# Optimization experiments

Hardware: AMD Instinct MI355X
Metric: run time of the kernel (lower is better)

## Reference

```python
import jax, jax.numpy as jnp
import numpy as np

B, N, M = 64, 4096, 128
TOTAL_LABELS = 21
TOTAL_POS = 128
TOTAL_NEG = 128
VARIANCES = jnp.array([0.1, 0.1, 0.2, 0.2], dtype=jnp.float32)


def _make_boxes(key, b, n):
    # valid [y1, x1, y2, x2] boxes in [0, 1]
    k1, k2 = jax.random.split(key)
    c1 = jax.random.uniform(k1, (b, n, 2), dtype=jnp.float32)
    c2 = jax.random.uniform(k2, (b, n, 2), dtype=jnp.float32)
    lo = jnp.minimum(c1, c2)
    hi = jnp.maximum(c1, c2)
    return jnp.concatenate([lo, hi], axis=-1)


def setup_inputs() -> dict:
    key = jax.random.key(0)
    k1, k2, k3 = jax.random.split(key, 3)
    roi_bboxes = _make_boxes(k1, B, N)
    gt_boxes = _make_boxes(k2, B, M)
    gt_labels = jax.random.randint(k3, (B, M), 0, TOTAL_LABELS, dtype=jnp.int32)
    return {"roi_bboxes": roi_bboxes, "gt_boxes": gt_boxes, "gt_labels": gt_labels}


def generate_iou(bboxes, gt_boxes):
    # bboxes: [B,N,4], gt_boxes: [B,M,4]; format [y1,x1,y2,x2] -> iou [B,N,M]
    by1, bx1, by2, bx2 = jnp.split(bboxes, 4, axis=-1)      # each [B,N,1]
    gy1, gx1, gy2, gx2 = jnp.split(gt_boxes, 4, axis=-1)    # each [B,M,1]
    gt_area = ((gy2 - gy1) * (gx2 - gx1))[..., 0]           # [B,M]
    bbox_area = ((by2 - by1) * (bx2 - bx1))[..., 0]         # [B,N]
    x_top = jnp.maximum(bx1, jnp.swapaxes(gx1, 1, 2))       # [B,N,M]
    y_top = jnp.maximum(by1, jnp.swapaxes(gy1, 1, 2))
    x_bot = jnp.minimum(bx2, jnp.swapaxes(gx2, 1, 2))
    y_bot = jnp.minimum(by2, jnp.swapaxes(gy2, 1, 2))
    inter = jnp.maximum(x_bot - x_top, 0.0) * jnp.maximum(y_bot - y_top, 0.0)
    union = bbox_area[:, :, None] + gt_area[:, None, :] - inter
    return inter / union


def randomly_select_mask(key, mask, count):
    # keep at most `count` True entries per row, chosen at random (rpn_utils.randomly_select_xyz_mask)
    rand = jax.random.randint(key, mask.shape, 1, count * 10, dtype=jnp.int32)
    mult = mask.astype(jnp.int32) * rand
    order = jnp.argsort(-mult, axis=1)       # descending sort of masked random scores
    rank = jnp.argsort(order, axis=1)        # rank of each element in that order
    return mask & (rank < count)


def bbox_to_delta(bboxes, gt_boxes):
    bw = bboxes[..., 3] - bboxes[..., 1]
    bh = bboxes[..., 2] - bboxes[..., 0]
    bcx = bboxes[..., 1] + 0.5 * bw
    bcy = bboxes[..., 0] + 0.5 * bh
    gw = gt_boxes[..., 3] - gt_boxes[..., 1]
    gh = gt_boxes[..., 2] - gt_boxes[..., 0]
    gcx = gt_boxes[..., 1] + 0.5 * gw
    gcy = gt_boxes[..., 0] + 0.5 * gh
    bw = jnp.where(bw == 0.0, 1e-3, bw)
    bh = jnp.where(bh == 0.0, 1e-3, bh)
    dx = (gcx - bcx) / bw
    dy = (gcy - bcy) / bh
    gw_safe = jnp.where(gw == 0.0, 1.0, gw)  # avoid nan grads through masked log
    gh_safe = jnp.where(gh == 0.0, 1.0, gh)
    dw = jnp.where(gw == 0.0, 0.0, jnp.log(gw_safe / bw))
    dh = jnp.where(gh == 0.0, 0.0, jnp.log(gh_safe / bh))
    return jnp.stack([dy, dx, dh, dw], axis=-1)


def _forward(roi_bboxes, gt_boxes, gt_labels):
    kp, kn = jax.random.split(jax.random.key(42))
    iou_map = generate_iou(roi_bboxes, gt_boxes)             # [B,N,M]
    max_idx = jnp.argmax(iou_map, axis=2)                    # [B,N]
    merged = jnp.max(iou_map, axis=2)                        # [B,N]
    pos_mask = randomly_select_mask(kp, merged > 0.5, TOTAL_POS)
    neg_mask = randomly_select_mask(kn, (merged < 0.5) & (merged > 0.1), TOTAL_NEG)
    # batched gather of best-matching gt box / label per roi
    gt_boxes_map = jnp.take_along_axis(gt_boxes, max_idx[..., None], axis=1)   # [B,N,4]
    gt_labels_map = jnp.take_along_axis(gt_labels, max_idx, axis=1)            # [B,N]
    expanded_gt_boxes = jnp.where(pos_mask[..., None], gt_boxes_map, 0.0)
    pos_gt_labels = jnp.where(pos_mask, gt_labels_map, -1)
    expanded_gt_labels = pos_gt_labels  # hyper_params['background'] == False
    deltas = bbox_to_delta(roi_bboxes, expanded_gt_boxes) / VARIANCES           # [B,N,4]
    labels_oh = jax.nn.one_hot(expanded_gt_labels, TOTAL_LABELS, dtype=deltas.dtype)  # [B,N,L]; -1 -> all zeros
    roi_bbox_deltas = labels_oh[..., None] * deltas[..., None, :]               # [B,N,L,4]
    return roi_bbox_deltas, labels_oh


def reference(roi_bboxes, gt_boxes, gt_labels):
    return _forward(roi_bboxes, gt_boxes, gt_labels)
```

## Files before the change

kernel.cpp:

```cpp
#include <hip/hip_runtime.h>
#include <stdint.h>

#pragma clang fp contract(off)


#define BB 64
#define NN 4096
#define MM 128
#define LL 21
#define NTOT (BB * NN)
#define DELTA_ELEMS ((size_t)BB * NN * LL * 4)

__host__ __device__ __forceinline__ uint32_t rotl32(uint32_t v, int s) {
  return (v << s) | (v >> (32 - s));
}

__host__ __device__ inline void threefry2x32(uint32_t k0, uint32_t k1,
                                             uint32_t x0, uint32_t x1,
                                             uint32_t* o0, uint32_t* o1) {
  const uint32_t ks2 = k0 ^ k1 ^ 0x1BD11BDAu;
  x0 += k0; x1 += k1;
#define TF_R(r) do { x0 += x1; x1 = rotl32(x1, (r)); x1 ^= x0; } while (0)
  TF_R(13); TF_R(15); TF_R(26); TF_R(6);
  x0 += k1;  x1 += ks2 + 1u;
  TF_R(17); TF_R(29); TF_R(16); TF_R(24);
  x0 += ks2; x1 += k0 + 2u;
  TF_R(13); TF_R(15); TF_R(26); TF_R(6);
  x0 += k0;  x1 += k1 + 3u;
  TF_R(17); TF_R(29); TF_R(16); TF_R(24);
  x0 += k1;  x1 += ks2 + 4u;
  TF_R(13); TF_R(15); TF_R(26); TF_R(6);
  x0 += ks2; x1 += k0 + 5u;
#undef TF_R
  *o0 = x0; *o1 = x1;
}

__device__ __forceinline__ uint32_t jax_bits32(uint32_t ka, uint32_t kb, uint32_t idx) {
  uint32_t o0, o1;
  threefry2x32(ka, kb, 0u, idx, &o0, &o1);
  return o0 ^ o1;
}

__device__ __forceinline__ uint32_t jax_randint_1_1280(uint32_t k1a, uint32_t k1b,
                                                       uint32_t k2a, uint32_t k2b,
                                                       uint32_t idx) {
  const uint32_t hi = jax_bits32(k1a, k1b, idx);
  const uint32_t lo = jax_bits32(k2a, k2b, idx);
  const uint32_t off = ((hi % 1279u) * 882u + (lo % 1279u)) % 1279u;
  return 1u + off;
}

__device__ __forceinline__ float4 compute_delta(const float4 r, const float4 g) {
  float bh = r.z - r.x, bw = r.w - r.y;
  const float bcy = r.x + 0.5f * bh, bcx = r.y + 0.5f * bw;
  const float gh = g.z - g.x, gw = g.w - g.y;
  const float gcy = g.x + 0.5f * gh, gcx = g.y + 0.5f * gw;
  if (bw == 0.0f) bw = 1e-3f;
  if (bh == 0.0f) bh = 1e-3f;
  const float dx = (gcx - bcx) / bw;
  const float dy = (gcy - bcy) / bh;
  const float dw = (gw == 0.0f) ? 0.0f : logf(gw / bw);
  const float dh = (gh == 0.0f) ? 0.0f : logf(gh / bh);
  float4 dv;
  dv.x = dy / 0.1f; dv.y = dx / 0.1f; dv.z = dh / 0.2f; dv.w = dw / 0.2f;
  return dv;
}

__global__ __launch_bounds__(256) void iou_pack_kernel(
    const float* __restrict__ roi, const float* __restrict__ gt,
    uint32_t* __restrict__ packed,
    uint32_t k1a, uint32_t k1b, uint32_t k2a, uint32_t k2b) {
  __shared__ float4 gtb[MM];
  __shared__ float gar[MM];
  const int b = blockIdx.y;
  const int t = threadIdx.x;
  if (t < MM) {
    const float4 g = ((const float4*)gt)[b * MM + t];
    gtb[t] = g;
    gar[t] = (g.z - g.x) * (g.w - g.y);
  }
  __syncthreads();
  const int i = b * NN + blockIdx.x * 256 + t;
  const float4 r = ((const float4*)roi)[i];
  const float barea = (r.z - r.x) * (r.w - r.y);
  float best = -1.0f;
  int bm = 0;
  for (int m = 0; m < MM; ++m) {
    const float4 g = gtb[m];
    const float xt = fmaxf(r.y, g.y);
    const float yt = fmaxf(r.x, g.x);
    const float xb = fminf(r.w, g.w);
    const float yb = fminf(r.z, g.z);
    const float inter = fmaxf(xb - xt, 0.0f) * fmaxf(yb - yt, 0.0f);
    const float uni = (barea + gar[m]) - inter;
    const float iou = inter / uni;
    if (iou > best) { best = iou; bm = m; }
  }
  const uint32_t rnd = jax_randint_1_1280(k1a, k1b, k2a, k2b, (uint32_t)i);
  packed[i] = (uint32_t)bm | ((best > 0.5f) ? (rnd << 7) : 0u);
}

__global__ __launch_bounds__(256) void fused_out_kernel(
    const float* __restrict__ roi, const float* __restrict__ gt,
    const int* __restrict__ glab, const uint32_t* __restrict__ packed,
    float* __restrict__ out) {
  __shared__ uint32_t hist[1280];
  __shared__ uint32_t scan[256];
  __shared__ unsigned char selb[NN];
  __shared__ float4 sdv[256];
  __shared__ int slbl[256];
  __shared__ int s_thr;
  __shared__ int s_take;
  const int br = blockIdx.x;
  const int b = br >> 4;
  const int win0 = (br & 15) << 8;
  const int t = threadIdx.x;
  for (int j = t; j < 1280; j += 256) hist[j] = 0u;
  if (t == 0) { s_thr = 0; s_take = 0; }
  __syncthreads();

  uint32_t rv[16];
  const uint4* p4 = (const uint4*)(packed + (size_t)b * NN);
  #pragma unroll
  for (int q = 0; q < 4; ++q) {
    const uint4 w = p4[t * 4 + q];
    rv[q * 4 + 0] = w.x >> 7;
    rv[q * 4 + 1] = w.y >> 7;
    rv[q * 4 + 2] = w.z >> 7;
    rv[q * 4 + 3] = w.w >> 7;
  }
  #pragma unroll
  for (int k = 0; k < 16; ++k)
    if (rv[k]) atomicAdd(&hist[rv[k]], 1u);
  __syncthreads();

  uint32_t chunk = 0;
  #pragma unroll
  for (int j = 0; j < 5; ++j) chunk += hist[t * 5 + j];
  scan[t] = chunk;
  __syncthreads();
  for (int off = 1; off < 256; off <<= 1) {
    const uint32_t v = (t + off < 256) ? scan[t + off] : 0u;
    __syncthreads();
    scan[t] += v;
    __syncthreads();
  }
  const uint32_t total = scan[0];
  if (total > 128u) {
    const uint32_t Sc = scan[t];
    const uint32_t Sn = (t < 255) ? scan[t + 1] : 0u;
    if (Sc >= 128u && Sn < 128u) {
      uint32_t s = Sn;
      #pragma unroll
      for (int j = 4; j >= 0; --j) {
        const uint32_t h = hist[t * 5 + j];
        if (s + h >= 128u) { s_thr = t * 5 + j; s_take = 128 - (int)s; break; }
        s += h;
      }
    }
  }
  __syncthreads();
  const uint32_t thr = (uint32_t)s_thr;
  const uint32_t take = (uint32_t)s_take;

  uint32_t lt = 0;
  if (thr > 0) {
    #pragma unroll
    for (int k = 0; k < 16; ++k) lt += (rv[k] == thr) ? 1u : 0u;
  }
  scan[t] = lt;
  __syncthreads();
  for (int off = 1; off < 256; off <<= 1) {
    const uint32_t v = (t >= off) ? scan[t - off] : 0u;
    __syncthreads();
    scan[t] += v;
    __syncthreads();
  }
  uint32_t run = scan[t] - lt;
  uint32_t sw0 = 0, sw1 = 0, sw2 = 0, sw3 = 0;
  #pragma unroll
  for (int k = 0; k < 16; ++k) {
    bool s;
    if (thr == 0) {
      s = rv[k] > 0u;
    } else {
      s = (rv[k] > thr);
      if (rv[k] == thr) { s = (run < take); ++run; }
    }
    const uint32_t bit = s ? 1u : 0u;
    if (k < 4)       sw0 |= bit << (k * 8);
    else if (k < 8)  sw1 |= bit << ((k - 4) * 8);
    else if (k < 12) sw2 |= bit << ((k - 8) * 8);
    else             sw3 |= bit << ((k - 12) * 8);
  }
  ((uint4*)selb)[t] = make_uint4(sw0, sw1, sw2, sw3);
  __syncthreads();

  const int irow = win0 + t;
  const int i = b * NN + irow;
  float4 dv = {0.f, 0.f, 0.f, 0.f};
  int lbl = -1;
  if (selb[irow]) {
    const int mi = (int)(packed[i] & 127u);
    const float4 r = ((const float4*)roi)[i];
    const float4 g = ((const float4*)gt)[b * MM + mi];
    lbl = glab[b * MM + mi];
    dv = compute_delta(r, g);
  }
  sdv[t] = dv;
  slbl[t] = lbl;
  __syncthreads();
  const float4 z = {0.f, 0.f, 0.f, 0.f};
  const size_t ri0 = (size_t)b * NN + win0;
  float4* dbase = (float4*)out + ri0 * LL;
  #pragma unroll
  for (int k = 0; k < LL; ++k) {
    const int q = t + k * 256;
    const int r = q / 21;
    const int f = q - r * 21;
    dbase[q] = (f == slbl[r]) ? sdv[r] : z;
  }
  float4* lbase = (float4*)(out + DELTA_ELEMS) + ri0 * LL / 4;
  for (int q = t; q < 1344; q += 256) {
    const int e0 = q * 4;
    float4 v;
    const int r0 = e0 / 21;       v.x = ((e0 - r0 * 21) == slbl[r0]) ? 1.f : 0.f;
    const int r1 = (e0 + 1) / 21; v.y = ((e0 + 1 - r1 * 21) == slbl[r1]) ? 1.f : 0.f;
    const int r2 = (e0 + 2) / 21; v.z = ((e0 + 2 - r2 * 21) == slbl[r2]) ? 1.f : 0.f;
    const int r3 = (e0 + 3) / 21; v.w = ((e0 + 3 - r3 * 21) == slbl[r3]) ? 1.f : 0.f;
    lbase[q] = v;
  }
}

__global__ __launch_bounds__(256) void iou_kernel_s(const float* __restrict__ roi,
                                                    const float* __restrict__ gt,
                                                    int* __restrict__ midx,
                                                    float* __restrict__ merged) {
  __shared__ float4 gtb[MM];
  __shared__ float gar[MM];
  const int b = blockIdx.y;
  const int t = threadIdx.x;
  if (t < MM) {
    const float4 g = ((const float4*)gt)[b * MM + t];
    gtb[t] = g;
    gar[t] = (g.z - g.x) * (g.w - g.y);
  }
  __syncthreads();
  const int i = b * NN + blockIdx.x * 256 + t;
  const float4 r = ((const float4*)roi)[i];
  const float barea = (r.z - r.x) * (r.w - r.y);
  float best = -1.0f;
  int bm = 0;
  for (int m = 0; m < MM; ++m) {
    const float4 g = gtb[m];
    const float xt = fmaxf(r.y, g.y);
    const float yt = fmaxf(r.x, g.x);
    const float xb = fminf(r.w, g.w);
    const float yb = fminf(r.z, g.z);
    const float inter = fmaxf(xb - xt, 0.0f) * fmaxf(yb - yt, 0.0f);
    const float iou = inter / ((barea + gar[m]) - inter);
    if (iou > best) { best = iou; bm = m; }
  }
  midx[(size_t)i * 84] = bm;
  merged[(size_t)i * 84] = best;
}

__global__ __launch_bounds__(256) void select_kernel_s(const float* __restrict__ merged,
                                                       int* __restrict__ sel,
                                                       uint32_t k1a, uint32_t k1b,
                                                       uint32_t k2a, uint32_t k2b) {
  __shared__ uint32_t buf[NN];
  __shared__ uint32_t hist[1280];
  __shared__ uint32_t scan[256];
  __shared__ int s_thr;
  __shared__ int s_take;
  const int b = blockIdx.x;
  const int t = threadIdx.x;
  for (int j = t; j < 1280; j += 256) hist[j] = 0u;
  if (t == 0) { s_thr = 0; s_take = 0; }
  #pragma unroll
  for (int k = 0; k < 16; ++k) {
    const int li = t + k * 256;
    buf[li] = __float_as_uint(merged[(size_t)(b * NN + li) * 84]);
  }
  __syncthreads();
  uint32_t rv[16];
  const int lbase = t * 16;
  #pragma unroll
  for (int k = 0; k < 16; ++k) {
    const int li = lbase + k;
    uint32_t r = 0u;
    if (__uint_as_float(buf[li]) > 0.5f) {
      r = jax_randint_1_1280(k1a, k1b, k2a, k2b, (uint32_t)(b * NN + li));
      atomicAdd(&hist[r], 1u);
    }
    rv[k] = r;
  }
  __syncthreads();
  uint32_t chunk = 0;
  #pragma unroll
  for (int j = 0; j < 5; ++j) chunk += hist[t * 5 + j];
  scan[t] = chunk;
  __syncthreads();
  for (int off = 1; off < 256; off <<= 1) {
    const uint32_t v = (t + off < 256) ? scan[t + off] : 0u;
    __syncthreads();
    scan[t] += v;
    __syncthreads();
  }
  const uint32_t total = scan[0];
  if (total > 128u) {
    const uint32_t Sc = scan[t];
    const uint32_t Sn = (t < 255) ? scan[t + 1] : 0u;
    if (Sc >= 128u && Sn < 128u) {
      uint32_t s = Sn;
      #pragma unroll
      for (int j = 4; j >= 0; --j) {
        const uint32_t h = hist[t * 5 + j];
        if (s + h >= 128u) { s_thr = t * 5 + j; s_take = 128 - (int)s; break; }
        s += h;
      }
    }
  }
  __syncthreads();
  const int thr = s_thr;
  const uint32_t take = (uint32_t)s_take;
  uint32_t lt = 0;
  if (thr > 0) {
    #pragma unroll
    for (int k = 0; k < 16; ++k) lt += (rv[k] == (uint32_t)thr) ? 1u : 0u;
  }
  scan[t] = lt;
  __syncthreads();
  for (int off = 1; off < 256; off <<= 1) {
    const uint32_t v = (t >= off) ? scan[t - off] : 0u;
    __syncthreads();
    scan[t] += v;
    __syncthreads();
  }
  uint32_t run = scan[t] - lt;
  #pragma unroll
  for (int k = 0; k < 16; ++k) {
    bool s;
    if (thr == 0) {
      s = rv[k] > 0u;
    } else {
      s = (rv[k] > (uint32_t)thr);
      if (rv[k] == (uint32_t)thr) { s = (run < take); ++run; }
    }
    buf[lbase + k] = s ? 1u : 0u;
  }
  __syncthreads();
  #pragma unroll
  for (int k = 0; k < 16; ++k) {
    const int li = t + k * 256;
    sel[(size_t)(b * NN + li) * 84] = (int)buf[li];
  }
}

__global__ __launch_bounds__(256) void out_kernel_s(const float* __restrict__ roi,
                                                    const float* __restrict__ gt,
                                                    const int* __restrict__ glab,
                                                    const int* __restrict__ midx,
                                                    const int* __restrict__ sel,
                                                    float* __restrict__ out) {
  __shared__ float4 sdv[256];
  __shared__ int slbl[256];
  const int t = threadIdx.x;
  const int ri0 = blockIdx.x * 256;
  const int i = ri0 + t;
  const int b = i >> 12;
  const int mi = midx[(size_t)i * 84];
  const int sv = sel[(size_t)i * 84];
  float4 dv = {0.f, 0.f, 0.f, 0.f};
  int lbl = -1;
  if (sv) {
    const float4 r = ((const float4*)roi)[i];
    const float4 g = ((const float4*)gt)[b * MM + mi];
    lbl = glab[b * MM + mi];
    dv = compute_delta(r, g);
  }
  sdv[t] = dv;
  slbl[t] = lbl;
  __syncthreads();
  const float4 z = {0.f, 0.f, 0.f, 0.f};
  float4* dbase = (float4*)out + (size_t)ri0 * LL;
  #pragma unroll
  for (int k = 0; k < LL; ++k) {
    const int q = t + k * 256;
    const int r = q / 21;
    const int f = q - r * 21;
    dbase[q] = (f == slbl[r]) ? sdv[r] : z;
  }
  float4* lbase = (float4*)(out + DELTA_ELEMS) + (size_t)ri0 * LL / 4;
  for (int q = t; q < 1344; q += 256) {
    const int e0 = q * 4;
    float4 v;
    const int r0 = e0 / 21;       v.x = ((e0 - r0 * 21) == slbl[r0]) ? 1.f : 0.f;
    const int r1 = (e0 + 1) / 21; v.y = ((e0 + 1 - r1 * 21) == slbl[r1]) ? 1.f : 0.f;
    const int r2 = (e0 + 2) / 21; v.z = ((e0 + 2 - r2 * 21) == slbl[r2]) ? 1.f : 0.f;
    const int r3 = (e0 + 3) / 21; v.w = ((e0 + 3 - r3 * 21) == slbl[r3]) ? 1.f : 0.f;
    lbase[q] = v;
  }
}

extern "C" void kernel_launch(void* const* d_in, const int* in_sizes, int n_in,
                              void* d_out, int out_size, void* d_ws, size_t ws_size,
                              hipStream_t stream) {
  const float* roi = (const float*)d_in[0];
  const float* gt  = (const float*)d_in[1];
  const int* glab  = (const int*)d_in[2];
  float* out = (float*)d_out;

  uint32_t kp0, kp1, k1a, k1b, k2a, k2b;
  threefry2x32(0u, 42u, 0u, 0u, &kp0, &kp1);
  threefry2x32(kp0, kp1, 0u, 0u, &k1a, &k1b);
  threefry2x32(kp0, kp1, 0u, 1u, &k2a, &k2b);

  if (d_ws != nullptr && ws_size >= (size_t)NTOT * 4) {
    uint32_t* packed = (uint32_t*)d_ws;
    hipLaunchKernelGGL(iou_pack_kernel, dim3(NN / 256, BB), dim3(256), 0, stream,
                       roi, gt, packed, k1a, k1b, k2a, k2b);
    hipLaunchKernelGGL(fused_out_kernel, dim3(NTOT / 256), dim3(256), 0, stream,
                       roi, gt, glab, packed, out);
  } else {
    int* midx     = (int*)out;
    float* merged = out + 1;
    int* sel      = (int*)out + 2;
    hipLaunchKernelGGL(iou_kernel_s, dim3(NN / 256, BB), dim3(256), 0, stream,
                       roi, gt, midx, merged);
    hipLaunchKernelGGL(select_kernel_s, dim3(BB), dim3(256), 0, stream,
                       merged, sel, k1a, k1b, k2a, k2b);
    hipLaunchKernelGGL(out_kernel_s, dim3(NTOT / 256), dim3(256), 0, stream,
                       roi, gt, glab, midx, sel, out);
  }
}
```

Before: 57.52 us.

## Use wavefront shuffle scans and hoist loads and delta compute in fused kernel

The two shared-memory Hillis-Steele scans in the selection kernel, each with a barrier at every step, become wavefront shuffle scans plus a small per-wave combine, which cuts the number of block-wide barriers. Global loads of the packed words, the roi, the gt box and the label are issued at kernel start and the delta is computed for every row before selection, so the memory latency overlaps the histogram phase. In the IoU kernels the gt area is recomputed in registers instead of being read from a shared array, and the inner loop is unrolled. The cost is extra arithmetic for rows that end up unselected, plus extra gather loads for those rows.

```diff
diff --git a/kernel.cpp b/kernel.cpp
--- a/kernel.cpp
+++ b/kernel.cpp
@@ -71,29 +71,25 @@
     uint32_t* __restrict__ packed,
     uint32_t k1a, uint32_t k1b, uint32_t k2a, uint32_t k2b) {
   __shared__ float4 gtb[MM];
-  __shared__ float gar[MM];
   const int b = blockIdx.y;
   const int t = threadIdx.x;
-  if (t < MM) {
-    const float4 g = ((const float4*)gt)[b * MM + t];
-    gtb[t] = g;
-    gar[t] = (g.z - g.x) * (g.w - g.y);
-  }
-  __syncthreads();
   const int i = b * NN + blockIdx.x * 256 + t;
   const float4 r = ((const float4*)roi)[i];
+  if (t < MM) gtb[t] = ((const float4*)gt)[b * MM + t];
+  __syncthreads();
   const float barea = (r.z - r.x) * (r.w - r.y);
   float best = -1.0f;
   int bm = 0;
+  #pragma unroll 4
   for (int m = 0; m < MM; ++m) {
     const float4 g = gtb[m];
+    const float garea = (g.z - g.x) * (g.w - g.y);
     const float xt = fmaxf(r.y, g.y);
     const float yt = fmaxf(r.x, g.x);
     const float xb = fminf(r.w, g.w);
     const float yb = fminf(r.z, g.z);
     const float inter = fmaxf(xb - xt, 0.0f) * fmaxf(yb - yt, 0.0f);
-    const float uni = (barea + gar[m]) - inter;
-    const float iou = inter / uni;
+    const float iou = inter / ((barea + garea) - inter);
     if (iou > best) { best = iou; bm = m; }
   }
   const uint32_t rnd = jax_randint_1_1280(k1a, k1b, k2a, k2b, (uint32_t)i);
@@ -105,7 +101,8 @@
     const int* __restrict__ glab, const uint32_t* __restrict__ packed,
     float* __restrict__ out) {
   __shared__ uint32_t hist[1280];
-  __shared__ uint32_t scan[256];
+  __shared__ uint32_t scan[257];
+  __shared__ uint32_t wsum[4];
   __shared__ unsigned char selb[NN];
   __shared__ float4 sdv[256];
   __shared__ int slbl[256];
@@ -115,40 +112,62 @@
   const int b = br >> 4;
   const int win0 = (br & 15) << 8;
   const int t = threadIdx.x;
+  const int lane = t & 63;
+  const int wid = t >> 6;
+
+  const int irow = win0 + t;
+  const int i = b * NN + irow;
+  const uint32_t pk_own = packed[i];
+  const uint4* p4 = (const uint4*)(packed + (size_t)b * NN);
+  const uint4 w0 = p4[t * 4 + 0];
+  const uint4 w1 = p4[t * 4 + 1];
+  const uint4 w2 = p4[t * 4 + 2];
+  const uint4 w3 = p4[t * 4 + 3];
+  const float4 r = ((const float4*)roi)[i];
+
   for (int j = t; j < 1280; j += 256) hist[j] = 0u;
-  if (t == 0) { s_thr = 0; s_take = 0; }
+  if (t == 0) { s_thr = 0; s_take = 0; scan[256] = 0u; }
   __syncthreads();
 
   uint32_t rv[16];
-  const uint4* p4 = (const uint4*)(packed + (size_t)b * NN);
-  #pragma unroll
-  for (int q = 0; q < 4; ++q) {
-    const uint4 w = p4[t * 4 + q];
-    rv[q * 4 + 0] = w.x >> 7;
-    rv[q * 4 + 1] = w.y >> 7;
-    rv[q * 4 + 2] = w.z >> 7;
-    rv[q * 4 + 3] = w.w >> 7;
-  }
+  rv[0] = w0.x >> 7;  rv[1] = w0.y >> 7;  rv[2] = w0.z >> 7;  rv[3] = w0.w >> 7;
+  rv[4] = w1.x >> 7;  rv[5] = w1.y >> 7;  rv[6] = w1.z >> 7;  rv[7] = w1.w >> 7;
+  rv[8] = w2.x >> 7;  rv[9] = w2.y >> 7;  rv[10] = w2.z >> 7; rv[11] = w2.w >> 7;
+  rv[12] = w3.x >> 7; rv[13] = w3.y >> 7; rv[14] = w3.z >> 7; rv[15] = w3.w >> 7;
   #pragma unroll
   for (int k = 0; k < 16; ++k)
     if (rv[k]) atomicAdd(&hist[rv[k]], 1u);
+
+  const int mi = (int)(pk_own & 127u);
+  const float4 g = ((const float4*)gt)[b * MM + mi];
+  int lbl = glab[b * MM + mi];
+  float4 dv = compute_delta(r, g);
   __syncthreads();
 
   uint32_t chunk = 0;
   #pragma unroll
   for (int j = 0; j < 5; ++j) chunk += hist[t * 5 + j];
-  scan[t] = chunk;
-  __syncthreads();
-  for (int off = 1; off < 256; off <<= 1) {
-    const uint32_t v = (t + off < 256) ? scan[t + off] : 0u;
-    __syncthreads();
-    scan[t] += v;
-    __syncthreads();
-  }
+  uint32_t v = chunk;
+  #pragma unroll
+  for (int off = 1; off < 64; off <<= 1) {
+    const uint32_t u = __shfl_down(v, off);
+    if (lane + off < 64) v += u;
+  }
+  if (lane == 0) wsum[wid] = v;
+  __syncthreads();
+  {
+    uint32_t add = 0;
+    #pragma unroll
+    for (int w = 0; w < 4; ++w)
+      if (w > wid) add += wsum[w];
+    v += add;
+  }
+  scan[t] = v;
+  __syncthreads();
   const uint32_t total = scan[0];
   if (total > 128u) {
-    const uint32_t Sc = scan[t];
-    const uint32_t Sn = (t < 255) ? scan[t + 1] : 0u;
+    const uint32_t Sc = v;
+    const uint32_t Sn = scan[t + 1];
     if (Sc >= 128u && Sn < 128u) {
       uint32_t s = Sn;
       #pragma unroll
@@ -168,15 +187,19 @@
     #pragma unroll
     for (int k = 0; k < 16; ++k) lt += (rv[k] == thr) ? 1u : 0u;
   }
-  scan[t] = lt;
-  __syncthreads();
-  for (int off = 1; off < 256; off <<= 1) {
-    const uint32_t v = (t >= off) ? scan[t - off] : 0u;
-    __syncthreads();
-    scan[t] += v;
-    __syncthreads();
-  }
-  uint32_t run = scan[t] - lt;
+  uint32_t p = lt;
+  #pragma unroll
+  for (int off = 1; off < 64; off <<= 1) {
+    const uint32_t u = __shfl_up(p, off);
+    if (lane >= off) p += u;
+  }
+  if (lane == 63) wsum[wid] = p;
+  __syncthreads();
+  uint32_t run = p - lt;
+  #pragma unroll
+  for (int w = 0; w < 4; ++w)
+    if (w < wid) run += wsum[w];
+
   uint32_t sw0 = 0, sw1 = 0, sw2 = 0, sw3 = 0;
   #pragma unroll
   for (int k = 0; k < 16; ++k) {
@@ -196,17 +219,7 @@
   ((uint4*)selb)[t] = make_uint4(sw0, sw1, sw2, sw3);
   __syncthreads();
 
-  const int irow = win0 + t;
-  const int i = b * NN + irow;
-  float4 dv = {0.f, 0.f, 0.f, 0.f};
-  int lbl = -1;
-  if (selb[irow]) {
-    const int mi = (int)(packed[i] & 127u);
-    const float4 r = ((const float4*)roi)[i];
-    const float4 g = ((const float4*)gt)[b * MM + mi];
-    lbl = glab[b * MM + mi];
-    dv = compute_delta(r, g);
-  }
+  if (!selb[irow]) lbl = -1;
   sdv[t] = dv;
   slbl[t] = lbl;
   __syncthreads();
@@ -216,19 +229,19 @@
   #pragma unroll
   for (int k = 0; k < LL; ++k) {
     const int q = t + k * 256;
-    const int r = q / 21;
-    const int f = q - r * 21;
-    dbase[q] = (f == slbl[r]) ? sdv[r] : z;
+    const int rr = q / 21;
+    const int f = q - rr * 21;
+    dbase[q] = (f == slbl[rr]) ? sdv[rr] : z;
   }
   float4* lbase = (float4*)(out + DELTA_ELEMS) + ri0 * LL / 4;
   for (int q = t; q < 1344; q += 256) {
     const int e0 = q * 4;
-    float4 v;
-    const int r0 = e0 / 21;       v.x = ((e0 - r0 * 21) == slbl[r0]) ? 1.f : 0.f;
-    const int r1 = (e0 + 1) / 21; v.y = ((e0 + 1 - r1 * 21) == slbl[r1]) ? 1.f : 0.f;
-    const int r2 = (e0 + 2) / 21; v.z = ((e0 + 2 - r2 * 21) == slbl[r2]) ? 1.f : 0.f;
-    const int r3 = (e0 + 3) / 21; v.w = ((e0 + 3 - r3 * 21) == slbl[r3]) ? 1.f : 0.f;
-    lbase[q] = v;
+    float4 vv;
+    const int r0 = e0 / 21;       vv.x = ((e0 - r0 * 21) == slbl[r0]) ? 1.f : 0.f;
+    const int r1 = (e0 + 1) / 21; vv.y = ((e0 + 1 - r1 * 21) == slbl[r1]) ? 1.f : 0.f;
+    const int r2 = (e0 + 2) / 21; vv.z = ((e0 + 2 - r2 * 21) == slbl[r2]) ? 1.f : 0.f;
+    const int r3 = (e0 + 3) / 21; vv.w = ((e0 + 3 - r3 * 21) == slbl[r3]) ? 1.f : 0.f;
+    lbase[q] = vv;
   }
 }
 
@@ -237,14 +250,9 @@
                                                     int* __restrict__ midx,
                                                     float* __restrict__ merged) {
   __shared__ float4 gtb[MM];
-  __shared__ float gar[MM];
   const int b = blockIdx.y;
   const int t = threadIdx.x;
-  if (t < MM) {
-    const float4 g = ((const float4*)gt)[b * MM + t];
-    gtb[t] = g;
-    gar[t] = (g.z - g.x) * (g.w - g.y);
-  }
+  if (t < MM) gtb[t] = ((const float4*)gt)[b * MM + t];
   __syncthreads();
   const int i = b * NN + blockIdx.x * 256 + t;
   const float4 r = ((const float4*)roi)[i];
@@ -253,12 +261,13 @@
   int bm = 0;
   for (int m = 0; m < MM; ++m) {
     const float4 g = gtb[m];
+    const float garea = (g.z - g.x) * (g.w - g.y);
     const float xt = fmaxf(r.y, g.y);
     const float yt = fmaxf(r.x, g.x);
     const float xb = fminf(r.w, g.w);
     const float yb = fminf(r.z, g.z);
     const float inter = fmaxf(xb - xt, 0.0f) * fmaxf(yb - yt, 0.0f);
-    const float iou = inter / ((barea + gar[m]) - inter);
+    const float iou = inter / ((barea + garea) - inter);
     if (iou > best) { best = iou; bm = m; }
   }
   midx[(size_t)i * 84] = bm;
```

After: 57.58 us. Within noise of the previous version (+0.1%).

## Zero outputs in IoU kernel and scatter only selected rows per batch

Applied to the files above, without the earlier changes.

The IoU/pack kernel now also writes zeros over the whole delta and one-hot output regions, so the dense write overlaps with the IoU compute. The second kernel runs one block per batch, does the random selection once instead of 16 times, and scatters deltas and the 1.0 label only for the selected rows. This removes the redundant per-window histogram/select work and the dense masked output pass. The risk is that the scatter kernel has only 64 blocks. Any unselected row relies entirely on the earlier zero fill, which is ordered correctly on the same stream. The fallback IoU kernel now recomputes gt area inline rather than caching it in shared memory.

```diff
diff --git a/kernel.cpp b/kernel.cpp
--- a/kernel.cpp
+++ b/kernel.cpp
@@ -66,22 +66,34 @@
   return dv;
 }
 
-__global__ __launch_bounds__(256) void iou_pack_kernel(
+__global__ __launch_bounds__(256) void iou_zero_pack_kernel(
     const float* __restrict__ roi, const float* __restrict__ gt,
-    uint32_t* __restrict__ packed,
+    uint32_t* __restrict__ packed, float* __restrict__ out,
     uint32_t k1a, uint32_t k1b, uint32_t k2a, uint32_t k2b) {
   __shared__ float4 gtb[MM];
   __shared__ float gar[MM];
   const int b = blockIdx.y;
   const int t = threadIdx.x;
+  const int ri0 = blockIdx.x * 256;
+  const int i = b * NN + ri0 + t;
+  const float4 r = ((const float4*)roi)[i];
   if (t < MM) {
     const float4 g = ((const float4*)gt)[b * MM + t];
     gtb[t] = g;
     gar[t] = (g.z - g.x) * (g.w - g.y);
   }
   __syncthreads();
-  const int i = b * NN + blockIdx.x * 256 + t;
-  const float4 r = ((const float4*)roi)[i];
+
+  const float4 z = {0.f, 0.f, 0.f, 0.f};
+  const size_t gri0 = (size_t)b * NN + ri0;
+  float4* dbase = (float4*)out + gri0 * LL;
+  #pragma unroll
+  for (int k = 0; k < LL; ++k) dbase[t + k * 256] = z;
+  float4* lbase = (float4*)(out + DELTA_ELEMS) + gri0 * LL / 4;
+  #pragma unroll
+  for (int q = 0; q < 5; ++q) lbase[t + q * 256] = z;
+  if (t < 1344 - 5 * 256) lbase[t + 5 * 256] = z;
+
   const float barea = (r.z - r.x) * (r.w - r.y);
   float best = -1.0f;
   int bm = 0;
@@ -100,20 +112,15 @@
   packed[i] = (uint32_t)bm | ((best > 0.5f) ? (rnd << 7) : 0u);
 }
 
-__global__ __launch_bounds__(256) void fused_out_kernel(
+__global__ __launch_bounds__(256) void select_scatter_kernel(
     const float* __restrict__ roi, const float* __restrict__ gt,
     const int* __restrict__ glab, const uint32_t* __restrict__ packed,
     float* __restrict__ out) {
   __shared__ uint32_t hist[1280];
   __shared__ uint32_t scan[256];
-  __shared__ unsigned char selb[NN];
-  __shared__ float4 sdv[256];
-  __shared__ int slbl[256];
   __shared__ int s_thr;
   __shared__ int s_take;
-  const int br = blockIdx.x;
-  const int b = br >> 4;
-  const int win0 = (br & 15) << 8;
+  const int b = blockIdx.x;
   const int t = threadIdx.x;
   for (int j = t; j < 1280; j += 256) hist[j] = 0u;
   if (t == 0) { s_thr = 0; s_take = 0; }
@@ -177,7 +184,7 @@
     __syncthreads();
   }
   uint32_t run = scan[t] - lt;
-  uint32_t sw0 = 0, sw1 = 0, sw2 = 0, sw3 = 0;
+
   #pragma unroll
   for (int k = 0; k < 16; ++k) {
     bool s;
@@ -187,48 +194,16 @@
       s = (rv[k] > thr);
       if (rv[k] == thr) { s = (run < take); ++run; }
     }
-    const uint32_t bit = s ? 1u : 0u;
-    if (k < 4)       sw0 |= bit << (k * 8);
-    else if (k < 8)  sw1 |= bit << ((k - 4) * 8);
-    else if (k < 12) sw2 |= bit << ((k - 8) * 8);
-    else             sw3 |= bit << ((k - 12) * 8);
-  }
-  ((uint4*)selb)[t] = make_uint4(sw0, sw1, sw2, sw3);
-  __syncthreads();
-
-  const int irow = win0 + t;
-  const int i = b * NN + irow;
-  float4 dv = {0.f, 0.f, 0.f, 0.f};
-  int lbl = -1;
-  if (selb[irow]) {
-    const int mi = (int)(packed[i] & 127u);
-    const float4 r = ((const float4*)roi)[i];
-    const float4 g = ((const float4*)gt)[b * MM + mi];
-    lbl = glab[b * MM + mi];
-    dv = compute_delta(r, g);
-  }
-  sdv[t] = dv;
-  slbl[t] = lbl;
-  __syncthreads();
-  const float4 z = {0.f, 0.f, 0.f, 0.f};
-  const size_t ri0 = (size_t)b * NN + win0;
-  float4* dbase = (float4*)out + ri0 * LL;
-  #pragma unroll
-  for (int k = 0; k < LL; ++k) {
-    const int q = t + k * 256;
-    const int r = q / 21;
-    const int f = q - r * 21;
-    dbase[q] = (f == slbl[r]) ? sdv[r] : z;
-  }
-  float4* lbase = (float4*)(out + DELTA_ELEMS) + ri0 * LL / 4;
-  for (int q = t; q < 1344; q += 256) {
-    const int e0 = q * 4;
-    float4 v;
-    const int r0 = e0 / 21;       v.x = ((e0 - r0 * 21) == slbl[r0]) ? 1.f : 0.f;
-    const int r1 = (e0 + 1) / 21; v.y = ((e0 + 1 - r1 * 21) == slbl[r1]) ? 1.f : 0.f;
-    const int r2 = (e0 + 2) / 21; v.z = ((e0 + 2 - r2 * 21) == slbl[r2]) ? 1.f : 0.f;
-    const int r3 = (e0 + 3) / 21; v.w = ((e0 + 3 - r3 * 21) == slbl[r3]) ? 1.f : 0.f;
-    lbase[q] = v;
+    if (s) {
+      const int i = b * NN + t * 16 + k;
+      const int mi = (int)(packed[i] & 127u);
+      const float4 r = ((const float4*)roi)[i];
+      const float4 g = ((const float4*)gt)[b * MM + mi];
+      const int lbl = glab[b * MM + mi];
+      const float4 dv = compute_delta(r, g);
+      ((float4*)out)[(size_t)i * LL + lbl] = dv;
+      out[DELTA_ELEMS + (size_t)i * LL + lbl] = 1.0f;
+    }
   }
 }
 
@@ -237,14 +212,9 @@
                                                     int* __restrict__ midx,
                                                     float* __restrict__ merged) {
   __shared__ float4 gtb[MM];
-  __shared__ float gar[MM];
   const int b = blockIdx.y;
   const int t = threadIdx.x;
-  if (t < MM) {
-    const float4 g = ((const float4*)gt)[b * MM + t];
-    gtb[t] = g;
-    gar[t] = (g.z - g.x) * (g.w - g.y);
-  }
+  if (t < MM) gtb[t] = ((const float4*)gt)[b * MM + t];
   __syncthreads();
   const int i = b * NN + blockIdx.x * 256 + t;
   const float4 r = ((const float4*)roi)[i];
@@ -253,12 +223,13 @@
   int bm = 0;
   for (int m = 0; m < MM; ++m) {
     const float4 g = gtb[m];
+    const float garea = (g.z - g.x) * (g.w - g.y);
     const float xt = fmaxf(r.y, g.y);
     const float yt = fmaxf(r.x, g.x);
     const float xb = fminf(r.w, g.w);
     const float yb = fminf(r.z, g.z);
     const float inter = fmaxf(xb - xt, 0.0f) * fmaxf(yb - yt, 0.0f);
-    const float iou = inter / ((barea + gar[m]) - inter);
+    const float iou = inter / ((barea + garea) - inter);
     if (iou > best) { best = iou; bm = m; }
   }
   midx[(size_t)i * 84] = bm;
@@ -419,9 +390,9 @@
 
   if (d_ws != nullptr && ws_size >= (size_t)NTOT * 4) {
     uint32_t* packed = (uint32_t*)d_ws;
-    hipLaunchKernelGGL(iou_pack_kernel, dim3(NN / 256, BB), dim3(256), 0, stream,
-                       roi, gt, packed, k1a, k1b, k2a, k2b);
-    hipLaunchKernelGGL(fused_out_kernel, dim3(NTOT / 256), dim3(256), 0, stream,
+    hipLaunchKernelGGL(iou_zero_pack_kernel, dim3(NN / 256, BB), dim3(256), 0,
+                       stream, roi, gt, packed, out, k1a, k1b, k2a, k2b);
+    hipLaunchKernelGGL(select_scatter_kernel, dim3(BB), dim3(256), 0, stream,
                        roi, gt, glab, packed, out);
   } else {
     int* midx     = (int*)out;
```

New measurement: 62.03 us. 7.9% more time.
